# Kernel tuning notes

Measured on AMD Instinct MI355X. Metric: run time of the kernel, lower is better.

The kernel has to match this reference:

```python
import jax, jax.numpy as jnp
import numpy as np

B, T, C = 4, 4096, 512
H, KS = 8, 9
D = C // H
PAD = KS // 2


def setup_inputs() -> dict:
    key = jax.random.key(0)
    ks = jax.random.split(key, 9)
    s = 1.0 / np.sqrt(C)
    return {
        "x": jax.random.normal(ks[0], (B, T, C), jnp.float32),
        "Wq": jax.random.normal(ks[1], (C, C), jnp.float32) * s,
        "bq": jax.random.normal(ks[2], (C,), jnp.float32) * 0.01,
        "Wk": jax.random.normal(ks[3], (C, C), jnp.float32) * s,
        "bk": jax.random.normal(ks[4], (C,), jnp.float32) * 0.01,
        "Wv": jax.random.normal(ks[5], (C, C), jnp.float32) * s,
        "bv": jax.random.normal(ks[6], (C,), jnp.float32) * 0.01,
        "Wo": jax.random.normal(ks[7], (C, C), jnp.float32) * s,
        "bo": jax.random.normal(ks[8], (C,), jnp.float32) * 0.01,
    }


def reference(x, Wq, bq, Wk, bk, Wv, bv, Wo, bo):
    Bx, Tx, Cx = x.shape
    # projections (torch Linear: x @ W.T + b), split heads -> (B,H,T,D)
    q = (x @ Wq.T + bq).reshape(Bx, Tx, H, D).transpose(0, 2, 1, 3)
    k = (x @ Wk.T + bk).reshape(Bx, Tx, H, D).transpose(0, 2, 1, 3)
    v = (x @ Wv.T + bv).reshape(Bx, Tx, H, D).transpose(0, 2, 1, 3)
    # replicate-pad along time (matches F.pad mode='replicate')
    k_pad = jnp.pad(k, ((0, 0), (0, 0), (PAD, PAD), (0, 0)), mode='edge')
    v_pad = jnp.pad(v, ((0, 0), (0, 0), (PAD, PAD), (0, 0)), mode='edge')
    # window gather indices: (T, KS) into padded time axis
    idx = jnp.arange(Tx)[:, None] + jnp.arange(KS)[None, :]
    k_unf = k_pad[:, :, idx, :]  # (B,H,T,KS,D)
    v_unf = v_pad[:, :, idx, :]  # (B,H,T,KS,D)
    scale = 1.0 / np.sqrt(D)
    scores = jnp.einsum('bhtd,bhtkd->bhtk', q, k_unf) * scale  # (B,H,T,KS)
    attn = jax.nn.softmax(scores, axis=-1)
    y = jnp.einsum('bhtk,bhtkd->bhtd', attn, v_unf)  # (B,H,T,D)
    y = y.transpose(0, 2, 1, 3).reshape(Bx, Tx, Cx)
    return y @ Wo.T + bo
```

## Files before the change

### kernel.cpp

```cpp
#include <hip/hip_runtime.h>
#include <hip/hip_bf16.h>

#define B_    4
#define T_    4096
#define C_    512
#define H_    8
#define D_    64
#define KS_   9
#define PAD_  4
#define MTOT  (B_ * T_)
#define PLANE (MTOT * C_)
#define XU    (MTOT * C_ / 8)
#define WU    (C_ * C_ / 8)

typedef __bf16 bf16_t;
typedef __bf16 bf16x8 __attribute__((ext_vector_type(8)));
typedef float  f32x4  __attribute__((ext_vector_type(4)));

__global__ __launch_bounds__(256)
void conv_all(const float* __restrict__ x,  const float* __restrict__ Wq,
              const float* __restrict__ Wk, const float* __restrict__ Wv,
              const float* __restrict__ Wo, bf16_t* __restrict__ dst) {
  int i = blockIdx.x * 256 + threadIdx.x;
  const float* s;
  if (i < XU) {
    s = x + (size_t)i * 8;
  } else {
    int r = i - XU;
    int w = r >> 15;
    const float* W = (w == 0) ? Wq : (w == 1) ? Wk : (w == 2) ? Wv : Wo;
    s = W + (size_t)(r & (WU - 1)) * 8;
  }
  float4 f0 = ((const float4*)s)[0];
  float4 f1 = ((const float4*)s)[1];
  bf16x8 o;
  o[0] = (bf16_t)f0.x; o[1] = (bf16_t)f0.y; o[2] = (bf16_t)f0.z; o[3] = (bf16_t)f0.w;
  o[4] = (bf16_t)f1.x; o[5] = (bf16_t)f1.y; o[6] = (bf16_t)f1.z; o[7] = (bf16_t)f1.w;
  ((bf16x8*)dst)[i] = o;
}

template <bool APLANE>
__device__ __forceinline__ void gemm_main(const bf16_t* __restrict__ A,
                                          const bf16_t* __restrict__ W,
                                          int m0, int n0, f32x4 acc[4][4]) {
  constexpr int K = C_;
  __shared__ __align__(16) bf16_t lsA[128 * 32];
  __shared__ __align__(16) bf16_t lsB[128 * 32];

  const int tid  = threadIdx.x;
  const int lane = tid & 63;
  const int wave = tid >> 6;
  const int wm   = (wave >> 1) * 64;
  const int wn   = (wave & 1) * 64;

  for (int k0 = 0; k0 < K; k0 += 32) {
    __syncthreads();
#pragma unroll
    for (int s = 0; s < 2; ++s) {
      int u   = s * 256 + tid;
      int row = u >> 2;
      int kp  = (u & 3) << 3;
      const bf16_t* ga;
      if (APLANE) {
        int m = m0 + row;
        int b = m >> 12, t = m & (T_ - 1);
        int h = k0 >> 6, d0 = (k0 & 63) + kp;
        ga = A + (((size_t)(b * H_ + h) * T_ + t) * D_ + d0);
      } else {
        ga = A + ((size_t)(m0 + row) * K + (k0 + kp));
      }
      const bf16_t* gb = W + ((size_t)(n0 + row) * K + (k0 + kp));
      __builtin_amdgcn_global_load_lds(
          (const __attribute__((address_space(1))) unsigned int*)ga,
          (__attribute__((address_space(3))) unsigned int*)&lsA[u * 8], 16, 0, 0);
      __builtin_amdgcn_global_load_lds(
          (const __attribute__((address_space(1))) unsigned int*)gb,
          (__attribute__((address_space(3))) unsigned int*)&lsB[u * 8], 16, 0, 0);
    }
    __syncthreads();

    const int kq = (lane >> 4) << 3;
    const int rr = lane & 15;
    bf16x8 af[4], bfr[4];
#pragma unroll
    for (int i = 0; i < 4; ++i) {
      af[i]  = *(const bf16x8*)&lsA[(wm + i * 16 + rr) * 32 + kq];
      bfr[i] = *(const bf16x8*)&lsB[(wn + i * 16 + rr) * 32 + kq];
    }
#pragma unroll
    for (int i = 0; i < 4; ++i)
#pragma unroll
      for (int j = 0; j < 4; ++j)
        acc[i][j] = __builtin_amdgcn_mfma_f32_16x16x32_bf16(af[i], bfr[j],
                                                            acc[i][j], 0, 0, 0);
  }
}

__global__ __launch_bounds__(256, 2)
void qkv_gemm(const bf16_t* __restrict__ xb, const bf16_t* __restrict__ Wb,
              const float* __restrict__ bq, const float* __restrict__ bk,
              const float* __restrict__ bv, bf16_t* __restrict__ qkv) {
  const int z  = blockIdx.z;
  const int m0 = blockIdx.y * 128, n0 = blockIdx.x * 128;
  f32x4 acc[4][4] = {};
  gemm_main<false>(xb, Wb + (size_t)z * C_ * C_, m0, n0, acc);

  const float* bias = (z == 0) ? bq : (z == 1) ? bk : bv;
  const int tid = threadIdx.x, lane = tid & 63, wave = tid >> 6;
  const int wm = (wave >> 1) * 64, wn = (wave & 1) * 64;
  const int cn = lane & 15, rb = (lane >> 4) << 2;

  float bvals[4];
#pragma unroll
  for (int j = 0; j < 4; ++j) bvals[j] = bias[n0 + wn + j * 16 + cn];

  const int bb = m0 >> 12;
  const int hh = (n0 + wn) >> 6;
  bf16_t* hb = qkv + (size_t)z * PLANE + (size_t)(bb * H_ + hh) * T_ * D_;
#pragma unroll
  for (int i = 0; i < 4; ++i) {
#pragma unroll
    for (int r = 0; r < 4; ++r) {
      int t = (m0 + wm + i * 16 + rb + r) & (T_ - 1);
      bf16_t* row = hb + (size_t)t * D_;
#pragma unroll
      for (int j = 0; j < 4; ++j)
        row[j * 16 + cn] = (bf16_t)(acc[i][j][r] + bvals[j]);
    }
  }
}

__global__ __launch_bounds__(256, 2)
void out_gemm(const bf16_t* __restrict__ y, const bf16_t* __restrict__ Wob,
              const float* __restrict__ bo, float* __restrict__ out) {
  const int m0 = blockIdx.y * 128, n0 = blockIdx.x * 128;
  f32x4 acc[4][4] = {};
  gemm_main<true>(y, Wob, m0, n0, acc);

  const int tid = threadIdx.x, lane = tid & 63, wave = tid >> 6;
  const int wm = (wave >> 1) * 64, wn = (wave & 1) * 64;
  const int cn = lane & 15, rb = (lane >> 4) << 2;
  float bvals[4];
#pragma unroll
  for (int j = 0; j < 4; ++j) bvals[j] = bo[n0 + wn + j * 16 + cn];
#pragma unroll
  for (int i = 0; i < 4; ++i) {
#pragma unroll
    for (int r = 0; r < 4; ++r) {
      int gm = m0 + wm + i * 16 + rb + r;
      float* orow = out + (size_t)gm * C_ + (n0 + wn);
#pragma unroll
      for (int j = 0; j < 4; ++j)
        orow[j * 16 + cn] = acc[i][j][r] + bvals[j];
    }
  }
}

__global__ __launch_bounds__(256)
void attn_kernel(const bf16_t* __restrict__ qkv, bf16_t* __restrict__ y) {
  const int tid  = threadIdx.x;
  const int sub  = tid & 7;
  const int tl   = tid >> 3;
  const int t    = blockIdx.x * 32 + tl;
  const int h    = blockIdx.y;
  const int b    = blockIdx.z;

  const size_t pl = (size_t)(b * H_ + h) * T_ * D_;
  const bf16_t* q = qkv + pl;
  const bf16_t* k = qkv + (size_t)PLANE + pl;
  const bf16_t* v = qkv + (size_t)2 * PLANE + pl;
  const int c = sub * 8;

  int tj[KS_];
#pragma unroll
  for (int j = 0; j < KS_; ++j) {
    int tt = t - PAD_ + j;
    tj[j] = tt < 0 ? 0 : (tt >= T_ ? T_ - 1 : tt);
  }

  bf16x8 q8 = *(const bf16x8*)(q + (size_t)t * D_ + c);
  float qf[8];
#pragma unroll
  for (int e = 0; e < 8; ++e) qf[e] = (float)q8[e];

  float s[KS_];
#pragma unroll
  for (int j = 0; j < KS_; ++j) {
    bf16x8 k8 = *(const bf16x8*)(k + (size_t)tj[j] * D_ + c);
    float d0 = 0.f;
#pragma unroll
    for (int e = 0; e < 8; ++e) d0 += qf[e] * (float)k8[e];
    s[j] = d0;
  }

#pragma unroll
  for (int m = 1; m < 8; m <<= 1)
#pragma unroll
    for (int j = 0; j < KS_; ++j) s[j] += __shfl_xor(s[j], m, 8);

  float mx = s[0];
#pragma unroll
  for (int j = 1; j < KS_; ++j) mx = fmaxf(mx, s[j]);
  float w[KS_], sum = 0.f;
#pragma unroll
  for (int j = 0; j < KS_; ++j) {
    w[j] = __expf((s[j] - mx) * 0.125f);
    sum += w[j];
  }
  const float inv = 1.f / sum;
#pragma unroll
  for (int j = 0; j < KS_; ++j) w[j] *= inv;

  float o[8] = {0.f, 0.f, 0.f, 0.f, 0.f, 0.f, 0.f, 0.f};
#pragma unroll
  for (int j = 0; j < KS_; ++j) {
    bf16x8 v8 = *(const bf16x8*)(v + (size_t)tj[j] * D_ + c);
#pragma unroll
    for (int e = 0; e < 8; ++e) o[e] += w[j] * (float)v8[e];
  }
  bf16x8 o8;
#pragma unroll
  for (int e = 0; e < 8; ++e) o8[e] = (bf16_t)o[e];
  *(bf16x8*)(y + pl + (size_t)t * D_ + c) = o8;
}

extern "C" void kernel_launch(void* const* d_in, const int* in_sizes, int n_in,
                              void* d_out, int out_size, void* d_ws, size_t ws_size,
                              hipStream_t stream) {
  const float* x  = (const float*)d_in[0];
  const float* Wq = (const float*)d_in[1];
  const float* bq = (const float*)d_in[2];
  const float* Wk = (const float*)d_in[3];
  const float* bk = (const float*)d_in[4];
  const float* Wv = (const float*)d_in[5];
  const float* bv = (const float*)d_in[6];
  const float* Wo = (const float*)d_in[7];
  const float* bo = (const float*)d_in[8];
  float* out = (float*)d_out;

  bf16_t* xb  = (bf16_t*)d_ws;
  bf16_t* Wb  = xb + (size_t)MTOT * C_;
  bf16_t* qkv = Wb + (size_t)4 * C_ * C_;
  bf16_t* y   = qkv + (size_t)3 * PLANE;

  conv_all<<<(XU + 4 * WU) / 256, 256, 0, stream>>>(x, Wq, Wk, Wv, Wo, xb);
  qkv_gemm<<<dim3(C_ / 128, MTOT / 128, 3), 256, 0, stream>>>(
      xb, Wb, bq, bk, bv, qkv);
  attn_kernel<<<dim3(T_ / 32, H_, B_), 256, 0, stream>>>(qkv, y);
  out_gemm<<<dim3(C_ / 128, MTOT / 128, 1), 256, 0, stream>>>(
      y, Wb + (size_t)3 * C_ * C_, bo, out);
}
```

Measured before the change: 176.2 us.

## Fuse x bf16 conversion into QKV GEMM and compute Q,K,V per block

Removes the separate fp32-to-bf16 pass over x: the QKV GEMM now loads fp32 x directly, converts it in registers and stores it to LDS. Each block computes all three projections against one shared A tile, so x is read once instead of three times. LDS tiles gain an XOR swizzle to cut bank conflicts. In exchange the block holds three times as many accumulators (192 floats per thread), which raises register pressure and may lower occupancy, and the A path no longer uses async global-to-LDS loads.

New measurement: 169.3 us. 3.9% less time.

```diff
diff --git a/kernel.cpp b/kernel.cpp
--- a/kernel.cpp
+++ b/kernel.cpp
@@ -10,7 +10,6 @@
 #define PAD_  4
 #define MTOT  (B_ * T_)
 #define PLANE (MTOT * C_)
-#define XU    (MTOT * C_ / 8)
 #define WU    (C_ * C_ / 8)
 
 typedef __bf16 bf16_t;
@@ -18,19 +17,13 @@
 typedef float  f32x4  __attribute__((ext_vector_type(4)));
 
 __global__ __launch_bounds__(256)
-void conv_all(const float* __restrict__ x,  const float* __restrict__ Wq,
-              const float* __restrict__ Wk, const float* __restrict__ Wv,
-              const float* __restrict__ Wo, bf16_t* __restrict__ dst) {
+void conv_w(const float* __restrict__ Wq, const float* __restrict__ Wk,
+            const float* __restrict__ Wv, const float* __restrict__ Wo,
+            bf16_t* __restrict__ dst) {
   int i = blockIdx.x * 256 + threadIdx.x;
-  const float* s;
-  if (i < XU) {
-    s = x + (size_t)i * 8;
-  } else {
-    int r = i - XU;
-    int w = r >> 15;
-    const float* W = (w == 0) ? Wq : (w == 1) ? Wk : (w == 2) ? Wv : Wo;
-    s = W + (size_t)(r & (WU - 1)) * 8;
-  }
+  int w = i >> 15;
+  const float* W = (w == 0) ? Wq : (w == 1) ? Wk : (w == 2) ? Wv : Wo;
+  const float* s = W + (size_t)(i & (WU - 1)) * 8;
   float4 f0 = ((const float4*)s)[0];
   float4 f1 = ((const float4*)s)[1];
   bf16x8 o;
@@ -39,37 +32,133 @@
   ((bf16x8*)dst)[i] = o;
 }
 
-template <bool APLANE>
-__device__ __forceinline__ void gemm_main(const bf16_t* __restrict__ A,
-                                          const bf16_t* __restrict__ W,
-                                          int m0, int n0, f32x4 acc[4][4]) {
-  constexpr int K = C_;
+__global__ __launch_bounds__(256, 2)
+void qkv_gemm(const float* __restrict__ x, const bf16_t* __restrict__ Wb,
+              const float* __restrict__ bq, const float* __restrict__ bk,
+              const float* __restrict__ bv, bf16_t* __restrict__ qkv) {
   __shared__ __align__(16) bf16_t lsA[128 * 32];
-  __shared__ __align__(16) bf16_t lsB[128 * 32];
+  __shared__ __align__(16) bf16_t lsB[3][128 * 32];
 
   const int tid  = threadIdx.x;
   const int lane = tid & 63;
   const int wave = tid >> 6;
   const int wm   = (wave >> 1) * 64;
   const int wn   = (wave & 1) * 64;
-
-  for (int k0 = 0; k0 < K; k0 += 32) {
-    __syncthreads();
+  const int m0   = blockIdx.y * 128;
+  const int n0   = blockIdx.x * 128;
+
+  f32x4 acc[3][4][4] = {};
+
+  for (int k0 = 0; k0 < C_; k0 += 32) {
+    bf16x8 a[2];
 #pragma unroll
     for (int s = 0; s < 2; ++s) {
-      int u   = s * 256 + tid;
-      int row = u >> 2;
-      int kp  = (u & 3) << 3;
-      const bf16_t* ga;
-      if (APLANE) {
-        int m = m0 + row;
-        int b = m >> 12, t = m & (T_ - 1);
-        int h = k0 >> 6, d0 = (k0 & 63) + kp;
-        ga = A + (((size_t)(b * H_ + h) * T_ + t) * D_ + d0);
-      } else {
-        ga = A + ((size_t)(m0 + row) * K + (k0 + kp));
+      int u = s * 256 + tid;
+      int row = u >> 2, slot = u & 3;
+      int c = slot ^ ((row >> 1) & 3);
+      const float* src = x + (size_t)(m0 + row) * C_ + k0 + c * 8;
+      float4 f0 = ((const float4*)src)[0];
+      float4 f1 = ((const float4*)src)[1];
+      a[s][0] = (bf16_t)f0.x; a[s][1] = (bf16_t)f0.y;
+      a[s][2] = (bf16_t)f0.z; a[s][3] = (bf16_t)f0.w;
+      a[s][4] = (bf16_t)f1.x; a[s][5] = (bf16_t)f1.y;
+      a[s][6] = (bf16_t)f1.z; a[s][7] = (bf16_t)f1.w;
+    }
+
+    __syncthreads();
+    *(bf16x8*)&lsA[(size_t)tid * 8]         = a[0];
+    *(bf16x8*)&lsA[(size_t)(tid + 256) * 8] = a[1];
+#pragma unroll
+    for (int z = 0; z < 3; ++z)
+#pragma unroll
+      for (int s = 0; s < 2; ++s) {
+        int u = s * 256 + tid;
+        int row = u >> 2, slot = u & 3;
+        int c = slot ^ ((row >> 1) & 3);
+        const bf16_t* gb = Wb + (size_t)z * C_ * C_ +
+                           (size_t)(n0 + row) * C_ + k0 + c * 8;
+        __builtin_amdgcn_global_load_lds(
+            (const __attribute__((address_space(1))) unsigned int*)gb,
+            (__attribute__((address_space(3))) unsigned int*)&lsB[z][u * 8],
+            16, 0, 0);
       }
-      const bf16_t* gb = W + ((size_t)(n0 + row) * K + (k0 + kp));
+    __syncthreads();
+
+    const int rr = lane & 15;
+    const int q  = lane >> 4;
+    const int sl = (q ^ ((rr >> 1) & 3)) << 3;
+    bf16x8 af[4];
+#pragma unroll
+    for (int i = 0; i < 4; ++i)
+      af[i] = *(const bf16x8*)&lsA[(wm + i * 16 + rr) * 32 + sl];
+#pragma unroll
+    for (int z = 0; z < 3; ++z) {
+      bf16x8 bfr[4];
+#pragma unroll
+      for (int j = 0; j < 4; ++j)
+        bfr[j] = *(const bf16x8*)&lsB[z][(wn + j * 16 + rr) * 32 + sl];
+#pragma unroll
+      for (int i = 0; i < 4; ++i)
+#pragma unroll
+        for (int j = 0; j < 4; ++j)
+          acc[z][i][j] = __builtin_amdgcn_mfma_f32_16x16x32_bf16(
+              af[i], bfr[j], acc[z][i][j], 0, 0, 0);
+    }
+  }
+
+  const int cn = lane & 15;
+  const int rb = (lane >> 4) << 2;
+  const int bb = m0 >> 12;
+  const int hh = (n0 + wn) >> 6;
+#pragma unroll
+  for (int z = 0; z < 3; ++z) {
+    const float* bias = (z == 0) ? bq : (z == 1) ? bk : bv;
+    float bvals[4];
+#pragma unroll
+    for (int j = 0; j < 4; ++j) bvals[j] = bias[n0 + wn + j * 16 + cn];
+    bf16_t* hb = qkv + (size_t)z * PLANE + (size_t)(bb * H_ + hh) * T_ * D_;
+#pragma unroll
+    for (int i = 0; i < 4; ++i) {
+#pragma unroll
+      for (int r = 0; r < 4; ++r) {
+        int t = (m0 + wm + i * 16 + rb + r) & (T_ - 1);
+        bf16_t* row = hb + (size_t)t * D_;
+#pragma unroll
+        for (int j = 0; j < 4; ++j)
+          row[j * 16 + cn] = (bf16_t)(acc[z][i][j][r] + bvals[j]);
+      }
+    }
+  }
+}
+
+__global__ __launch_bounds__(256, 2)
+void out_gemm(const bf16_t* __restrict__ y, const bf16_t* __restrict__ Wob,
+              const float* __restrict__ bo, float* __restrict__ out) {
+  __shared__ __align__(16) bf16_t lsA[128 * 32];
+  __shared__ __align__(16) bf16_t lsB[128 * 32];
+
+  const int tid  = threadIdx.x;
+  const int lane = tid & 63;
+  const int wave = tid >> 6;
+  const int wm   = (wave >> 1) * 64;
+  const int wn   = (wave & 1) * 64;
+  const int m0   = blockIdx.y * 128;
+  const int n0   = blockIdx.x * 128;
+
+  f32x4 acc[4][4] = {};
+
+  for (int k0 = 0; k0 < C_; k0 += 32) {
+    __syncthreads();
+#pragma unroll
+    for (int s = 0; s < 2; ++s) {
+      int u = s * 256 + tid;
+      int row = u >> 2, slot = u & 3;
+      int c = slot ^ ((row >> 1) & 3);
+      int m = m0 + row;
+      int b = m >> 12, t = m & (T_ - 1);
+      int h = k0 >> 6, d0 = (k0 & 63) + c * 8;
+      const bf16_t* ga = y + (((size_t)(b * H_ + h) * T_ + t) * D_ + d0);
+      const bf16_t* gb = Wob + (size_t)(n0 + row) * C_ + k0 + c * 8;
       __builtin_amdgcn_global_load_lds(
           (const __attribute__((address_space(1))) unsigned int*)ga,
           (__attribute__((address_space(3))) unsigned int*)&lsA[u * 8], 16, 0, 0);
@@ -79,13 +168,14 @@
     }
     __syncthreads();
 
-    const int kq = (lane >> 4) << 3;
     const int rr = lane & 15;
+    const int q  = lane >> 4;
+    const int sl = (q ^ ((rr >> 1) & 3)) << 3;
     bf16x8 af[4], bfr[4];
 #pragma unroll
     for (int i = 0; i < 4; ++i) {
-      af[i]  = *(const bf16x8*)&lsA[(wm + i * 16 + rr) * 32 + kq];
-      bfr[i] = *(const bf16x8*)&lsB[(wn + i * 16 + rr) * 32 + kq];
+      af[i]  = *(const bf16x8*)&lsA[(wm + i * 16 + rr) * 32 + sl];
+      bfr[i] = *(const bf16x8*)&lsB[(wn + i * 16 + rr) * 32 + sl];
     }
 #pragma unroll
     for (int i = 0; i < 4; ++i)
@@ -94,52 +184,9 @@
         acc[i][j] = __builtin_amdgcn_mfma_f32_16x16x32_bf16(af[i], bfr[j],
                                                             acc[i][j], 0, 0, 0);
   }
-}
-
-__global__ __launch_bounds__(256, 2)
-void qkv_gemm(const bf16_t* __restrict__ xb, const bf16_t* __restrict__ Wb,
-              const float* __restrict__ bq, const float* __restrict__ bk,
-              const float* __restrict__ bv, bf16_t* __restrict__ qkv) {
-  const int z  = blockIdx.z;
-  const int m0 = blockIdx.y * 128, n0 = blockIdx.x * 128;
-  f32x4 acc[4][4] = {};
-  gemm_main<false>(xb, Wb + (size_t)z * C_ * C_, m0, n0, acc);
-
-  const float* bias = (z == 0) ? bq : (z == 1) ? bk : bv;
-  const int tid = threadIdx.x, lane = tid & 63, wave = tid >> 6;
-  const int wm = (wave >> 1) * 64, wn = (wave & 1) * 64;
-  const int cn = lane & 15, rb = (lane >> 4) << 2;
-
-  float bvals[4];
-#pragma unroll
-  for (int j = 0; j < 4; ++j) bvals[j] = bias[n0 + wn + j * 16 + cn];
-
-  const int bb = m0 >> 12;
-  const int hh = (n0 + wn) >> 6;
-  bf16_t* hb = qkv + (size_t)z * PLANE + (size_t)(bb * H_ + hh) * T_ * D_;
-#pragma unroll
-  for (int i = 0; i < 4; ++i) {
-#pragma unroll
-    for (int r = 0; r < 4; ++r) {
-      int t = (m0 + wm + i * 16 + rb + r) & (T_ - 1);
-      bf16_t* row = hb + (size_t)t * D_;
-#pragma unroll
-      for (int j = 0; j < 4; ++j)
-        row[j * 16 + cn] = (bf16_t)(acc[i][j][r] + bvals[j]);
-    }
-  }
-}
-
-__global__ __launch_bounds__(256, 2)
-void out_gemm(const bf16_t* __restrict__ y, const bf16_t* __restrict__ Wob,
-              const float* __restrict__ bo, float* __restrict__ out) {
-  const int m0 = blockIdx.y * 128, n0 = blockIdx.x * 128;
-  f32x4 acc[4][4] = {};
-  gemm_main<true>(y, Wob, m0, n0, acc);
-
-  const int tid = threadIdx.x, lane = tid & 63, wave = tid >> 6;
-  const int wm = (wave >> 1) * 64, wn = (wave & 1) * 64;
-  const int cn = lane & 15, rb = (lane >> 4) << 2;
+
+  const int cn = lane & 15;
+  const int rb = (lane >> 4) << 2;
   float bvals[4];
 #pragma unroll
   for (int j = 0; j < 4; ++j) bvals[j] = bo[n0 + wn + j * 16 + cn];
@@ -238,14 +285,13 @@
   const float* bo = (const float*)d_in[8];
   float* out = (float*)d_out;
 
-  bf16_t* xb  = (bf16_t*)d_ws;
-  bf16_t* Wb  = xb + (size_t)MTOT * C_;
+  bf16_t* Wb  = (bf16_t*)d_ws;
   bf16_t* qkv = Wb + (size_t)4 * C_ * C_;
   bf16_t* y   = qkv + (size_t)3 * PLANE;
 
-  conv_all<<<(XU + 4 * WU) / 256, 256, 0, stream>>>(x, Wq, Wk, Wv, Wo, xb);
-  qkv_gemm<<<dim3(C_ / 128, MTOT / 128, 3), 256, 0, stream>>>(
-      xb, Wb, bq, bk, bv, qkv);
+  conv_w<<<4 * WU / 256, 256, 0, stream>>>(Wq, Wk, Wv, Wo, Wb);
+  qkv_gemm<<<dim3(C_ / 128, MTOT / 128), 256, 0, stream>>>(
+      x, Wb, bq, bk, bv, qkv);
   attn_kernel<<<dim3(T_ / 32, H_, B_), 256, 0, stream>>>(qkv, y);
   out_gemm<<<dim3(C_ / 128, MTOT / 128, 1), 256, 0, stream>>>(
       y, Wb + (size_t)3 * C_ * C_, bo, out);
```
